# Performance work log

Measured on AMD Instinct MI355X. Metric: run time of the kernel, lower is better.

Reference implementation:

```python
import jax, jax.numpy as jnp
import numpy as np

T, B, NN = 20, 4, 500            # timesteps, batch, nodes per sample
M = B * NN                        # big-batched node count = 2000
IN_D, H, H2, OUT = 2, 128, 64, 32


def setup_inputs() -> dict:
    key = jax.random.key(0)
    ks = jax.random.split(key, 16)
    positions = jax.random.normal(ks[0], (T, M, IN_D), jnp.float32)
    adjacency = (jax.random.uniform(ks[1], (T, M, M)) < 0.01).astype(jnp.float32)
    adjacency = adjacency * (1.0 - jnp.eye(M, dtype=jnp.float32))
    ego_mask = jax.random.bernoulli(ks[2], 0.8, (B, T, NN))
    s = lambda k, shp, fan: (jax.random.normal(k, shp, jnp.float32) / np.sqrt(fan)).astype(jnp.float32)
    return {
        'positions': positions,
        'adjacency': adjacency,
        'ego_mask': ego_mask,
        'W1': s(ks[3], (IN_D, H), IN_D), 'b1': jnp.zeros((H,), jnp.float32),
        'W2': s(ks[4], (H, H), H),       'b2': jnp.zeros((H,), jnp.float32),
        'W_ih': s(ks[5], (4 * H, H), H), 'W_hh': s(ks[6], (4 * H, H), H),
        'b_ih': jnp.zeros((4 * H,), jnp.float32), 'b_hh': jnp.zeros((4 * H,), jnp.float32),
        'fc1_w': s(ks[7], (H, H2), H),   'fc1_b': jnp.zeros((H2,), jnp.float32),
        'fc2_w': s(ks[8], (H2, OUT), H2), 'fc2_b': jnp.zeros((OUT,), jnp.float32),
    }


def _forward(positions, adjacency, ego_mask, W1, b1, W2, b2,
             W_ih, W_hh, b_ih, b_hh, fc1_w, fc1_b, fc2_w, fc2_b):
    # ego_mask [B,T,NN] -> [T, B*NN] (matches permute(1,0,2).reshape(T,-1))
    mask = jnp.transpose(ego_mask, (1, 0, 2)).reshape(T, M).astype(positions.dtype)

    def gcn_timestep(x_t, a_t, m_t):
        # masked subgraph + self loops on kept nodes (PyG GCNConv normalization)
        Ahat = a_t * m_t[:, None] * m_t[None, :] + jnp.diag(m_t)   # [M,M]
        deg = Ahat.sum(axis=0)                                      # in-degree (col sum)
        dinv = jnp.where(deg > 0, jax.lax.rsqrt(jnp.maximum(deg, 1e-12)), 0.0)
        An = dinv[:, None] * Ahat * dinv[None, :]                   # D^-1/2 Ahat D^-1/2
        h1 = jax.nn.relu(An.T @ (x_t @ W1) + b1)                    # GCN1 + relu
        h2 = (An.T @ (h1 @ W2) + b2) * m_t[:, None]                 # GCN2, scatter into zeros
        return h2

    placeholder = jax.vmap(gcn_timestep)(positions, adjacency, mask)  # [T, M, H]

    # torch nn.LSTM (batch_first=False) on placeholder.transpose(0,1):
    # sequence axis = nodes (M), batch axis = T
    xs = jnp.transpose(placeholder, (1, 0, 2))  # [M, T, H]

    def lstm_step(carry, x_s):
        h, c = carry
        gates = x_s @ W_ih.T + b_ih + h @ W_hh.T + b_hh
        i, f, g, o = jnp.split(gates, 4, axis=-1)
        c = jax.nn.sigmoid(f) * c + jax.nn.sigmoid(i) * jnp.tanh(g)
        h = jax.nn.sigmoid(o) * jnp.tanh(c)
        return (h, c), h

    init = (jnp.zeros((T, H), positions.dtype), jnp.zeros((T, H), positions.dtype))
    _, lstm_out = jax.lax.scan(lstm_step, init, xs)  # [M, T, H]

    emb = lstm_out.reshape(B, NN, T, H)              # view(B, max_nodes, T, H)
    emb = jax.nn.relu(emb @ fc1_w + fc1_b)
    return emb @ fc2_w + fc2_b                       # [B, NN, T, OUT]


def reference(positions, adjacency, ego_mask, W1, b1, W2, b2,
              W_ih, W_hh, b_ih, b_hh, fc1_w, fc1_b, fc2_w, fc2_b):
    return _forward(positions, adjacency, ego_mask, W1, b1, W2, b2,
                    W_ih, W_hh, b_ih, b_hh, fc1_w, fc1_b, fc2_w, fc2_b)
```

## Files before the change

### kernel.cpp

```cpp
#include <hip/hip_runtime.h>
#include <hip/hip_bf16.h>

#define T_   20
#define B_   4
#define NN_  500
#define M_   2000
#define TM_  40000
#define H_   128
#define G_   512
#define H2_  64
#define OUT_ 32
#define ECAP 64
#define TG_  (T_ * G_)

typedef unsigned short ushort_t;
typedef unsigned int   uint_t;
typedef _Float16       f16;
typedef f16 f16x2 __attribute__((ext_vector_type(2)));
typedef f16 f16x8 __attribute__((ext_vector_type(8)));
typedef float f32x4 __attribute__((ext_vector_type(4)));

#if defined(__has_builtin)
#  if __has_builtin(__builtin_amdgcn_fdot2)
#    define HAVE_FDOT2 1
#  endif
#endif

__device__ inline float fdot2_(f16x2 a, f16x2 b, float c) {
#ifdef HAVE_FDOT2
    return __builtin_amdgcn_fdot2(a, b, c, false);
#else
    return c + (float)a.x * (float)b.x + (float)a.y * (float)b.y;
#endif
}

__device__ inline float fast_sig(float x) {
    float e = __builtin_amdgcn_exp2f(x * -1.4426950408889634f);
    return __builtin_amdgcn_rcpf(1.f + e);
}
__device__ inline float fast_tanh(float x) {
    float e = __builtin_amdgcn_exp2f(x * 2.8853900817779268f);
    return 1.f - 2.f * __builtin_amdgcn_rcpf(e + 1.f);
}

#define BARRAW() asm volatile("s_barrier" ::: "memory")

#define DPPADD(v, ctrl)                                                       \
    do {                                                                      \
        int nb_ = __builtin_amdgcn_update_dpp(                                \
            0, __builtin_bit_cast(int, v), (ctrl), 0xF, 0xF, true);           \
        v += __builtin_bit_cast(float, nb_);                                  \
    } while (0)

__global__ __launch_bounds__(1024) void k0_mask(const void* __restrict__ ego,
                                                float* __restrict__ mf,
                                                int* __restrict__ ecnt) {
    __shared__ int fl[3];
    int tid = threadIdx.x;
    if (tid < 3) fl[tid] = 0;
    __syncthreads();
    const uint_t* dw = (const uint_t*)ego;
    int a = 0, b = 0, c = 0;
    for (int i = tid; i < 2500; i += 1024) {
        uint_t v = dw[i];
        bool isf32  = (v == 0x3F800000u);
        bool isbf16 = (v == 0x00003F80u) || (v == 0x3F803F80u);
        if (isf32)  a = 1;
        if (isbf16) b = 1;
        if (v > 1u && !isf32 && !isbf16) c = 1;
    }
    if (a) fl[0] = 1;
    if (b) fl[1] = 1;
    if (c) fl[2] = 1;
    __syncthreads();
    int mode;
    if (fl[1])      mode = 3;
    else if (fl[0]) mode = 2;
    else if (fl[2]) mode = 1;
    else            mode = 0;
    int e = blockIdx.x * 1024 + tid;
    if (e >= TM_) return;
    ecnt[e] = 0;
    int t = e / M_, i = e % M_;
    int bb = i / NN_, n = i % NN_;
    int src = (bb * T_ + t) * NN_ + n;
    bool on;
    if (mode == 0)      on = ((const int*)ego)[src] != 0;
    else if (mode == 1) on = ((const unsigned char*)ego)[src] != 0;
    else if (mode == 2) on = ((const float*)ego)[src] != 0.f;
    else                on = ((const ushort_t*)ego)[src] != 0;
    mf[e] = on ? 1.f : 0.f;
}

#define JSTRIP 200
__global__ void k1_scan(const float* __restrict__ adj, const float* __restrict__ mf,
                        int* __restrict__ ecnt, int* __restrict__ edges) {
    __shared__ float ms[JSTRIP];
    int t = blockIdx.y, j0 = blockIdx.z * JSTRIP;
    int i = blockIdx.x * 256 + threadIdx.x;
    for (int idx = threadIdx.x; idx < JSTRIP; idx += 256)
        ms[idx] = mf[t * M_ + j0 + idx];
    __syncthreads();
    if (i >= M_) return;
    if (mf[t * M_ + i] == 0.f) return;
    const float* ap = adj + (size_t)t * M_ * M_ + (size_t)j0 * M_ + i;
    int r = t * M_ + i;
    int* ep = edges + (size_t)r * ECAP;
#pragma unroll 8
    for (int jj = 0; jj < JSTRIP; ++jj) {
        float av = ap[(size_t)jj * M_];
        if (av != 0.f && ms[jj] != 0.f) {
            int pos = atomicAdd(&ecnt[r], 1);
            if (pos < ECAP) ep[pos] = j0 + jj;
        }
    }
}

__global__ void k2_y1(const float* __restrict__ pos, const float* __restrict__ W1,
                      const float* __restrict__ mf, const int* __restrict__ ecnt,
                      float* __restrict__ dinv, f16* __restrict__ Y1) {
    int gid = blockIdx.x * 256 + threadIdx.x;
    int r = gid >> 7, h = gid & 127;
    if (r >= TM_) return;
    float mr = mf[r];
    int cnt = ecnt[r];
    float dv = (mr != 0.f) ? __frsqrt_rn((float)(cnt + 1)) : 0.f;
    if (h == 0) dinv[r] = dv;
    float2 xy = ((const float2*)pos)[r];
    float v = xy.x * W1[h] + xy.y * W1[H_ + h];
    Y1[gid] = (f16)(dv * v);
}

__global__ __launch_bounds__(64) void k3_agg1(const f16* __restrict__ Y1,
        const float* __restrict__ dinv, const int* __restrict__ ecnt,
        const int* __restrict__ edges, const float* __restrict__ b1,
        f16* __restrict__ h1) {
    int r = blockIdx.x, q = threadIdx.x;
    int t = r / M_, base = t * M_;
    const uint_t* Yu = (const uint_t*)Y1;
    f16x2 sp = __builtin_bit_cast(f16x2, Yu[(size_t)r * 64 + q]);
    float a0 = (float)sp.x, a1 = (float)sp.y;
    int ec = ecnt[r]; if (ec > ECAP) ec = ECAP;
    const int4* ep4 = (const int4*)(edges + (size_t)r * ECAP);
    for (int e = 0; e < ec; e += 4) {
        int4 ix = ep4[e >> 2];
        int j1 = (e + 1 < ec) ? ix.y : ix.x;
        int j2 = (e + 2 < ec) ? ix.z : ix.x;
        int j3 = (e + 3 < ec) ? ix.w : ix.x;
        uint_t u0 = Yu[(size_t)(base + ix.x) * 64 + q];
        uint_t u1 = Yu[(size_t)(base + j1) * 64 + q];
        uint_t u2 = Yu[(size_t)(base + j2) * 64 + q];
        uint_t u3 = Yu[(size_t)(base + j3) * 64 + q];
        f16x2 p0 = __builtin_bit_cast(f16x2, u0);
        a0 += (float)p0.x; a1 += (float)p0.y;
        if (e + 1 < ec) { f16x2 p = __builtin_bit_cast(f16x2, u1); a0 += (float)p.x; a1 += (float)p.y; }
        if (e + 2 < ec) { f16x2 p = __builtin_bit_cast(f16x2, u2); a0 += (float)p.x; a1 += (float)p.y; }
        if (e + 3 < ec) { f16x2 p = __builtin_bit_cast(f16x2, u3); a0 += (float)p.x; a1 += (float)p.y; }
    }
    float dv = dinv[r];
    float o0 = dv * a0 + b1[2 * q];
    float o1 = dv * a1 + b1[2 * q + 1];
    f16x2 op; op.x = (f16)fmaxf(o0, 0.f); op.y = (f16)fmaxf(o1, 0.f);
    ((uint_t*)h1)[(size_t)r * 64 + q] = __builtin_bit_cast(uint_t, op);
}

__global__ __launch_bounds__(64) void k5_agg2(const f16* __restrict__ Y2,
        const float* __restrict__ dinv, const float* __restrict__ mf,
        const int* __restrict__ ecnt, const int* __restrict__ edges,
        const float* __restrict__ b2, f16* __restrict__ ph) {
    int r = blockIdx.x, q = threadIdx.x;
    int t = r / M_, base = t * M_;
    const uint_t* Yu = (const uint_t*)Y2;
    f16x2 sp = __builtin_bit_cast(f16x2, Yu[(size_t)r * 64 + q]);
    float a0 = (float)sp.x, a1 = (float)sp.y;
    int ec = ecnt[r]; if (ec > ECAP) ec = ECAP;
    const int4* ep4 = (const int4*)(edges + (size_t)r * ECAP);
    for (int e = 0; e < ec; e += 4) {
        int4 ix = ep4[e >> 2];
        int j1 = (e + 1 < ec) ? ix.y : ix.x;
        int j2 = (e + 2 < ec) ? ix.z : ix.x;
        int j3 = (e + 3 < ec) ? ix.w : ix.x;
        uint_t u0 = Yu[(size_t)(base + ix.x) * 64 + q];
        uint_t u1 = Yu[(size_t)(base + j1) * 64 + q];
        uint_t u2 = Yu[(size_t)(base + j2) * 64 + q];
        uint_t u3 = Yu[(size_t)(base + j3) * 64 + q];
        f16x2 p0 = __builtin_bit_cast(f16x2, u0);
        a0 += (float)p0.x; a1 += (float)p0.y;
        if (e + 1 < ec) { f16x2 p = __builtin_bit_cast(f16x2, u1); a0 += (float)p.x; a1 += (float)p.y; }
        if (e + 2 < ec) { f16x2 p = __builtin_bit_cast(f16x2, u2); a0 += (float)p.x; a1 += (float)p.y; }
        if (e + 3 < ec) { f16x2 p = __builtin_bit_cast(f16x2, u3); a0 += (float)p.x; a1 += (float)p.y; }
    }
    float dv = dinv[r], mr = mf[r];
    f16x2 op;
    op.x = (f16)((dv * a0 + b2[2 * q]) * mr);
    op.y = (f16)((dv * a1 + b2[2 * q + 1]) * mr);
    ((uint_t*)ph)[(size_t)r * 64 + q] = __builtin_bit_cast(uint_t, op);
}

#define ALD 136
__global__ __launch_bounds__(256) void kgemm_mfma(const f16* __restrict__ A,
        const float* __restrict__ Bw, int bTrans, int Ntot, int mode,
        const float* __restrict__ dinv, const float* __restrict__ ba,
        const float* __restrict__ bb, f16* __restrict__ Out) {
    __shared__ f16 As[64 * ALD];
    __shared__ f16 Bs[64 * ALD];
    int m0 = blockIdx.x * 64;
    int n0 = blockIdx.y * 64;
    int tid = threadIdx.x;
#pragma unroll
    for (int u = 0; u < 4; ++u) {
        int idx = u * 256 + tid;
        int row = idx >> 4, seg = idx & 15;
        *(f16x8*)&As[row * ALD + seg * 8] =
            *(const f16x8*)(A + (size_t)(m0 + row) * H_ + seg * 8);
    }
    if (bTrans) {
#pragma unroll
        for (int u = 0; u < 16; ++u) {
            int idx = u * 256 + tid;
            int n = idx >> 6, k2 = (idx & 63) * 2;
            float2 v = *(const float2*)(Bw + (size_t)(n0 + n) * H_ + k2);
            f16x2 pk; pk.x = (f16)v.x; pk.y = (f16)v.y;
            *(uint_t*)&Bs[n * ALD + k2] = __builtin_bit_cast(uint_t, pk);
        }
    } else {
#pragma unroll
        for (int u = 0; u < 16; ++u) {
            int idx = u * 256 + tid;
            int n = idx >> 6, k2 = (idx & 63) * 2;
            f16x2 pk;
            pk.x = (f16)Bw[(size_t)k2 * Ntot + n0 + n];
            pk.y = (f16)Bw[(size_t)(k2 + 1) * Ntot + n0 + n];
            *(uint_t*)&Bs[n * ALD + k2] = __builtin_bit_cast(uint_t, pk);
        }
    }
    __syncthreads();
    int w = tid >> 6, lane = tid & 63;
    int col = lane & 15, quad = lane >> 4;
    f32x4 acc[4] = {};
#pragma unroll
    for (int kk = 0; kk < 4; ++kk) {
        f16x8 af = *(const f16x8*)&As[(w * 16 + col) * ALD + kk * 32 + quad * 8];
#pragma unroll
        for (int nt = 0; nt < 4; ++nt) {
            f16x8 bf = *(const f16x8*)&Bs[(nt * 16 + col) * ALD + kk * 32 + quad * 8];
            acc[nt] = __builtin_amdgcn_mfma_f32_16x16x32_f16(af, bf, acc[nt], 0, 0, 0);
        }
    }
    if (mode == 0) {
        float dv[4];
#pragma unroll
        for (int reg = 0; reg < 4; ++reg)
            dv[reg] = dinv[m0 + w * 16 + quad * 4 + reg];
#pragma unroll
        for (int nt = 0; nt < 4; ++nt) {
            int n = n0 + nt * 16 + col;
#pragma unroll
            for (int reg = 0; reg < 4; ++reg) {
                int r = m0 + w * 16 + quad * 4 + reg;
                Out[(size_t)r * Ntot + n] = (f16)(dv[reg] * acc[nt][reg]);
            }
        }
    } else {
#pragma unroll
        for (int nt = 0; nt < 4; ++nt) {
            int n = n0 + nt * 16 + col;
            float bias = ba[n] + bb[n];
            int pos = (n & 127) * 4 + (n >> 7);
#pragma unroll
            for (int reg = 0; reg < 4; ++reg) {
                int r = m0 + w * 16 + quad * 4 + reg;
                int t = r / M_, s = r % M_;
                Out[((size_t)s * T_ + t) * G_ + pos] = (f16)(acc[nt][reg] + bias);
            }
        }
    }
}

__global__ __launch_bounds__(512, 2) void k7_lstm(const float* __restrict__ Whh,
        const f16* __restrict__ xg, f16* __restrict__ lo) {
    __shared__ ushort_t hb2[2][H_];
    int t = blockIdx.x, tid = threadIdx.x;
    int m = tid >> 2, q = tid & 3;
    f16x2 wv[4][16];
#pragma unroll
    for (int gt = 0; gt < 4; ++gt) {
        const float* wr = Whh + (size_t)(gt * H_ + m) * H_ + q * 32;
#pragma unroll
        for (int d = 0; d < 16; ++d) {
            f16x2 p; p.x = (f16)wr[2 * d]; p.y = (f16)wr[2 * d + 1];
            wv[gt][d] = p;
        }
    }
    if (tid < H_) hb2[0][tid] = 0;
    float cst = 0.f;
    const ushort_t* xpu = (const ushort_t*)xg + t * G_ + m * 4 + q;
    ushort_t xa[8], xb[8];
#pragma unroll
    for (int k = 0; k < 8; ++k) xa[k] = xpu[(size_t)k * TG_];
    __syncthreads();

#define LSTM_STEP(S, XV)                                                      \
    do {                                                                      \
        const ushort_t* hp = &hb2[(S) & 1][q * 32];                           \
        uint4 u0 = ((const uint4*)hp)[0];                                     \
        uint4 u1 = ((const uint4*)hp)[1];                                     \
        uint4 u2 = ((const uint4*)hp)[2];                                     \
        uint4 u3 = ((const uint4*)hp)[3];                                     \
        uint_t hu[16] = {u0.x, u0.y, u0.z, u0.w, u1.x, u1.y, u1.z, u1.w,      \
                         u2.x, u2.y, u2.z, u2.w, u3.x, u3.y, u3.z, u3.w};     \
        float a0 = 0.f, a1 = 0.f, a2 = 0.f, a3 = 0.f;                         \
        _Pragma("unroll")                                                     \
        for (int d = 0; d < 16; ++d) {                                        \
            f16x2 e = __builtin_bit_cast(f16x2, hu[d]);                       \
            a0 = fdot2_(wv[0][d], e, a0);                                     \
            a1 = fdot2_(wv[1][d], e, a1);                                     \
            a2 = fdot2_(wv[2][d], e, a2);                                     \
            a3 = fdot2_(wv[3][d], e, a3);                                     \
        }                                                                     \
        float xf = (float)__builtin_bit_cast(f16, (ushort_t)(XV));            \
        a0 += (q == 0) ? xf : 0.f;                                            \
        a1 += (q == 1) ? xf : 0.f;                                            \
        a2 += (q == 2) ? xf : 0.f;                                            \
        a3 += (q == 3) ? xf : 0.f;                                            \
        DPPADD(a0, 0xB1); DPPADD(a0, 0x4E);                                   \
        DPPADD(a1, 0xB1); DPPADD(a1, 0x4E);                                   \
        DPPADD(a2, 0xB1); DPPADD(a2, 0x4E);                                   \
        DPPADD(a3, 0xB1); DPPADD(a3, 0x4E);                                   \
        float gi = fast_sig(a0), gf = fast_sig(a1);                           \
        float gg = fast_tanh(a2), go = fast_sig(a3);                          \
        cst = gf * cst + gi * gg;                                             \
        float hv_ = go * fast_tanh(cst);                                      \
        f16 hh = (f16)hv_;                                                    \
        if (q == 0) {                                                         \
            hb2[((S) & 1) ^ 1][m] = __builtin_bit_cast(ushort_t, hh);         \
            lo[((size_t)(S) * T_ + t) * H_ + m] = hh;                         \
        }                                                                     \
        BARRAW();                                                             \
    } while (0)

    for (int c2 = 0; c2 < 125; ++c2) {
        int s0 = c2 * 16;
#pragma unroll
        for (int k = 0; k < 8; ++k) xb[k] = xpu[(size_t)(s0 + 8 + k) * TG_];
#pragma unroll
        for (int k = 0; k < 8; ++k) LSTM_STEP(s0 + k, xa[k]);
        int nbs = (s0 + 16 <= M_ - 8) ? s0 + 16 : M_ - 8;
#pragma unroll
        for (int k = 0; k < 8; ++k) xa[k] = xpu[(size_t)(nbs + k) * TG_];
#pragma unroll
        for (int k = 0; k < 8; ++k) LSTM_STEP(s0 + 8 + k, xb[k]);
    }
#undef LSTM_STEP
}

__global__ __launch_bounds__(256) void k8_fc(const f16* __restrict__ lo,
        const float* __restrict__ w1, const float* __restrict__ fb1,
        const float* __restrict__ w2, const float* __restrict__ fb2,
        float* __restrict__ out) {
    __shared__ uint_t hl[4][H_ / 2];
    __shared__ float o1f[4][H2_];
    int tid = threadIdx.x;
    int o = tid & 63, rr = tid >> 6;
    f16x2 w1c[64];
#pragma unroll
    for (int d = 0; d < 64; ++d) {
        f16x2 p;
        p.x = (f16)w1[(2 * d) * H2_ + o];
        p.y = (f16)w1[(2 * d + 1) * H2_ + o];
        w1c[d] = p;
    }
    int o2 = o & 31;
    float w2f[64];
#pragma unroll
    for (int d = 0; d < 64; ++d) w2f[d] = w2[d * OUT_ + o2];
    float fb1v = fb1[o], fb2v = fb2[o2];

    for (int r0 = blockIdx.x * 4; r0 < TM_; r0 += 512 * 4) {
        {
            int row = tid >> 6, qq = tid & 63;
            hl[row][qq] = ((const uint_t*)lo)[(size_t)(r0 + row) * 64 + qq];
        }
        __syncthreads();
        float acc = fb1v;
        const uint4* hb = (const uint4*)&hl[rr][0];
#pragma unroll
        for (int d = 0; d < 16; ++d) {
            uint4 hv = hb[d];
            acc = fdot2_(w1c[4 * d + 0], __builtin_bit_cast(f16x2, hv.x), acc);
            acc = fdot2_(w1c[4 * d + 1], __builtin_bit_cast(f16x2, hv.y), acc);
            acc = fdot2_(w1c[4 * d + 2], __builtin_bit_cast(f16x2, hv.z), acc);
            acc = fdot2_(w1c[4 * d + 3], __builtin_bit_cast(f16x2, hv.w), acc);
        }
        o1f[rr][o] = fmaxf(acc, 0.f);
        __syncthreads();
        if (o < OUT_) {
            float a2 = fb2v;
            const float4* ob = (const float4*)&o1f[rr][0];
#pragma unroll
            for (int d = 0; d < 16; ++d) {
                float4 v = ob[d];
                a2 += v.x * w2f[4 * d + 0] + v.y * w2f[4 * d + 1]
                    + v.z * w2f[4 * d + 2] + v.w * w2f[4 * d + 3];
            }
            out[(size_t)(r0 + rr) * OUT_ + o] = a2;
        }
        __syncthreads();
    }
}

extern "C" void kernel_launch(void* const* d_in, const int* in_sizes, int n_in,
                              void* d_out, int out_size, void* d_ws, size_t ws_size,
                              hipStream_t stream) {
    const float* positions = (const float*)d_in[0];
    const float* adjacency = (const float*)d_in[1];
    const void*  ego       = d_in[2];
    const float* W1   = (const float*)d_in[3];
    const float* b1   = (const float*)d_in[4];
    const float* W2   = (const float*)d_in[5];
    const float* b2   = (const float*)d_in[6];
    const float* W_ih = (const float*)d_in[7];
    const float* W_hh = (const float*)d_in[8];
    const float* b_ih = (const float*)d_in[9];
    const float* b_hh = (const float*)d_in[10];
    const float* fc1w = (const float*)d_in[11];
    const float* fc1b = (const float*)d_in[12];
    const float* fc2w = (const float*)d_in[13];
    const float* fc2b = (const float*)d_in[14];
    float* out = (float*)d_out;

    char* p = (char*)d_ws;
    auto alloc = [&](size_t bytes) {
        void* r = (void*)p;
        p += (bytes + 255) & ~(size_t)255;
        return r;
    };
    float* mf    = (float*)alloc((size_t)TM_ * 4);
    float* dinv  = (float*)alloc((size_t)TM_ * 4);
    int*   ecnt  = (int*)alloc((size_t)TM_ * 4);
    int*   edges = (int*)alloc((size_t)TM_ * ECAP * 4);
    f16*   bufC  = (f16*)alloc((size_t)TM_ * H_ * 2);
    f16*   bufD  = (f16*)alloc((size_t)TM_ * H_ * 2);
    f16*   xg    = (f16*)alloc((size_t)TM_ * G_ * 2);
    f16*   Y1 = bufC, *Y2 = bufC;
    f16*   h1 = bufD, *ph = bufD;
    f16*   lo = (f16*)edges;

    hipLaunchKernelGGL(k0_mask, dim3(40), dim3(1024), 0, stream, ego, mf, ecnt);
    hipLaunchKernelGGL(k1_scan, dim3(8, 20, 10), dim3(256), 0, stream,
                       adjacency, mf, ecnt, edges);
    hipLaunchKernelGGL(k2_y1, dim3(20000), dim3(256), 0, stream,
                       positions, W1, mf, ecnt, dinv, Y1);
    hipLaunchKernelGGL(k3_agg1, dim3(40000), dim3(64), 0, stream,
                       Y1, dinv, ecnt, edges, b1, h1);
    hipLaunchKernelGGL(kgemm_mfma, dim3(625, 2), dim3(256), 0, stream,
                       h1, W2, 0, 128, 0, dinv, (const float*)nullptr,
                       (const float*)nullptr, Y2);
    hipLaunchKernelGGL(k5_agg2, dim3(40000), dim3(64), 0, stream,
                       Y2, dinv, mf, ecnt, edges, b2, ph);
    hipLaunchKernelGGL(kgemm_mfma, dim3(625, 8), dim3(256), 0, stream,
                       ph, W_ih, 1, 512, 1, dinv, b_ih, b_hh, xg);
    hipLaunchKernelGGL(k7_lstm, dim3(20), dim3(512), 0, stream, W_hh, xg, lo);
    hipLaunchKernelGGL(k8_fc, dim3(512), dim3(256), 0, stream,
                       lo, fc1w, fc1b, fc2w, fc2b, out);
}
```

Baseline: 1.776 ms.

## Halve LSTM block to 256 threads with each thread computing two hidden units

The sequential LSTM kernel now runs 256 threads per block instead of 512. Each thread holds twice as many W_hh rows in registers (8x16 f16x2) and computes dot products for two hidden units across all four gates. The x-gate input is loaded as a packed 4-gate uint2 per hidden unit rather than one scalar per thread. This is meant to shorten each serial timestep's barrier and synchronisation cost by using fewer waves. In exchange it raises register pressure and doubles the fdot2 work per thread on the critical path.

Result: faster. 1.638 ms, median of 2 (-7.8%).

```diff
diff --git a/kernel.cpp b/kernel.cpp
--- a/kernel.cpp
+++ b/kernel.cpp
@@ -277,32 +277,37 @@
     }
 }
 
-__global__ __launch_bounds__(512, 2) void k7_lstm(const float* __restrict__ Whh,
-        const f16* __restrict__ xg, f16* __restrict__ lo) {
+__global__ __launch_bounds__(256, 1)
+__attribute__((amdgpu_waves_per_eu(1, 1)))
+void k7_lstm(const float* __restrict__ Whh,
+             const f16* __restrict__ xg, f16* __restrict__ lo) {
     __shared__ ushort_t hb2[2][H_];
     int t = blockIdx.x, tid = threadIdx.x;
-    int m = tid >> 2, q = tid & 3;
-    f16x2 wv[4][16];
-#pragma unroll
-    for (int gt = 0; gt < 4; ++gt) {
-        const float* wr = Whh + (size_t)(gt * H_ + m) * H_ + q * 32;
+    int r = tid >> 2, c = tid & 3;
+    f16x2 wv[8][16];
+#pragma unroll
+    for (int j = 0; j < 8; ++j) {
+        const float* wr = Whh + (size_t)(r + 64 * j) * H_ + c * 32;
 #pragma unroll
         for (int d = 0; d < 16; ++d) {
             f16x2 p; p.x = (f16)wr[2 * d]; p.y = (f16)wr[2 * d + 1];
-            wv[gt][d] = p;
+            wv[j][d] = p;
         }
     }
     if (tid < H_) hb2[0][tid] = 0;
+    int hsel = (c < 2) ? r : r + 64;
+    bool wr0 = (c & 1) == 0;
     float cst = 0.f;
-    const ushort_t* xpu = (const ushort_t*)xg + t * G_ + m * 4 + q;
-    ushort_t xa[8], xb[8];
-#pragma unroll
-    for (int k = 0; k < 8; ++k) xa[k] = xpu[(size_t)k * TG_];
+    const uint_t* xbase = (const uint_t*)xg;
+    uint2 xa[4], xb[4];
+#pragma unroll
+    for (int k = 0; k < 4; ++k)
+        xa[k] = *(const uint2*)(xbase + ((size_t)k * T_ + t) * 256 + hsel * 2);
     __syncthreads();
 
 #define LSTM_STEP(S, XV)                                                      \
     do {                                                                      \
-        const ushort_t* hp = &hb2[(S) & 1][q * 32];                           \
+        const ushort_t* hp = &hb2[(S) & 1][c * 32];                           \
         uint4 u0 = ((const uint4*)hp)[0];                                     \
         uint4 u1 = ((const uint4*)hp)[1];                                     \
         uint4 u2 = ((const uint4*)hp)[2];                                     \
@@ -310,6 +315,7 @@
         uint_t hu[16] = {u0.x, u0.y, u0.z, u0.w, u1.x, u1.y, u1.z, u1.w,      \
                          u2.x, u2.y, u2.z, u2.w, u3.x, u3.y, u3.z, u3.w};     \
         float a0 = 0.f, a1 = 0.f, a2 = 0.f, a3 = 0.f;                         \
+        float a4 = 0.f, a5 = 0.f, a6 = 0.f, a7 = 0.f;                         \
         _Pragma("unroll")                                                     \
         for (int d = 0; d < 16; ++d) {                                        \
             f16x2 e = __builtin_bit_cast(f16x2, hu[d]);                       \
@@ -317,39 +323,52 @@
             a1 = fdot2_(wv[1][d], e, a1);                                     \
             a2 = fdot2_(wv[2][d], e, a2);                                     \
             a3 = fdot2_(wv[3][d], e, a3);                                     \
+            a4 = fdot2_(wv[4][d], e, a4);                                     \
+            a5 = fdot2_(wv[5][d], e, a5);                                     \
+            a6 = fdot2_(wv[6][d], e, a6);                                     \
+            a7 = fdot2_(wv[7][d], e, a7);                                     \
         }                                                                     \
-        float xf = (float)__builtin_bit_cast(f16, (ushort_t)(XV));            \
-        a0 += (q == 0) ? xf : 0.f;                                            \
-        a1 += (q == 1) ? xf : 0.f;                                            \
-        a2 += (q == 2) ? xf : 0.f;                                            \
-        a3 += (q == 3) ? xf : 0.f;                                            \
         DPPADD(a0, 0xB1); DPPADD(a0, 0x4E);                                   \
         DPPADD(a1, 0xB1); DPPADD(a1, 0x4E);                                   \
         DPPADD(a2, 0xB1); DPPADD(a2, 0x4E);                                   \
         DPPADD(a3, 0xB1); DPPADD(a3, 0x4E);                                   \
-        float gi = fast_sig(a0), gf = fast_sig(a1);                           \
-        float gg = fast_tanh(a2), go = fast_sig(a3);                          \
+        DPPADD(a4, 0xB1); DPPADD(a4, 0x4E);                                   \
+        DPPADD(a5, 0xB1); DPPADD(a5, 0x4E);                                   \
+        DPPADD(a6, 0xB1); DPPADD(a6, 0x4E);                                   \
+        DPPADD(a7, 0xB1); DPPADD(a7, 0x4E);                                   \
+        float vi = (c < 2) ? a0 : a1;                                         \
+        float vf = (c < 2) ? a2 : a3;                                         \
+        float vg = (c < 2) ? a4 : a5;                                         \
+        float vo = (c < 2) ? a6 : a7;                                         \
+        f16x2 xlo = __builtin_bit_cast(f16x2, (XV).x);                        \
+        f16x2 xhi = __builtin_bit_cast(f16x2, (XV).y);                        \
+        float gi = fast_sig(vi + (float)xlo.x);                               \
+        float gf = fast_sig(vf + (float)xlo.y);                               \
+        float gg = fast_tanh(vg + (float)xhi.x);                              \
+        float go = fast_sig(vo + (float)xhi.y);                               \
         cst = gf * cst + gi * gg;                                             \
         float hv_ = go * fast_tanh(cst);                                      \
         f16 hh = (f16)hv_;                                                    \
-        if (q == 0) {                                                         \
-            hb2[((S) & 1) ^ 1][m] = __builtin_bit_cast(ushort_t, hh);         \
-            lo[((size_t)(S) * T_ + t) * H_ + m] = hh;                         \
+        if (wr0) {                                                            \
+            hb2[((S) & 1) ^ 1][hsel] = __builtin_bit_cast(ushort_t, hh);      \
+            lo[((size_t)(S) * T_ + t) * H_ + hsel] = hh;                      \
         }                                                                     \
         BARRAW();                                                             \
     } while (0)
 
-    for (int c2 = 0; c2 < 125; ++c2) {
-        int s0 = c2 * 16;
-#pragma unroll
-        for (int k = 0; k < 8; ++k) xb[k] = xpu[(size_t)(s0 + 8 + k) * TG_];
-#pragma unroll
-        for (int k = 0; k < 8; ++k) LSTM_STEP(s0 + k, xa[k]);
-        int nbs = (s0 + 16 <= M_ - 8) ? s0 + 16 : M_ - 8;
-#pragma unroll
-        for (int k = 0; k < 8; ++k) xa[k] = xpu[(size_t)(nbs + k) * TG_];
-#pragma unroll
-        for (int k = 0; k < 8; ++k) LSTM_STEP(s0 + 8 + k, xb[k]);
+    for (int c2 = 0; c2 < 250; ++c2) {
+        int s0 = c2 * 8;
+#pragma unroll
+        for (int k = 0; k < 4; ++k)
+            xb[k] = *(const uint2*)(xbase + ((size_t)(s0 + 4 + k) * T_ + t) * 256 + hsel * 2);
+#pragma unroll
+        for (int k = 0; k < 4; ++k) LSTM_STEP(s0 + k, xa[k]);
+        int nbs = (s0 + 8 <= M_ - 4) ? s0 + 8 : M_ - 4;
+#pragma unroll
+        for (int k = 0; k < 4; ++k)
+            xa[k] = *(const uint2*)(xbase + ((size_t)(nbs + k) * T_ + t) * 256 + hsel * 2);
+#pragma unroll
+        for (int k = 0; k < 4; ++k) LSTM_STEP(s0 + 4 + k, xb[k]);
     }
 #undef LSTM_STEP
 }
@@ -460,7 +479,7 @@
                        Y2, dinv, mf, ecnt, edges, b2, ph);
     hipLaunchKernelGGL(kgemm_mfma, dim3(625, 8), dim3(256), 0, stream,
                        ph, W_ih, 1, 512, 1, dinv, b_ih, b_hh, xg);
-    hipLaunchKernelGGL(k7_lstm, dim3(20), dim3(512), 0, stream, W_hh, xg, lo);
+    hipLaunchKernelGGL(k7_lstm, dim3(20), dim3(256), 0, stream, W_hh, xg, lo);
     hipLaunchKernelGGL(k8_fc, dim3(512), dim3(256), 0, stream,
                        lo, fc1w, fc1b, fc2w, fc2b, out);
 }
```
